# Performance work log

Hardware: AMD Instinct MI355X
Metric: run time of the kernel (lower is better)

## Reference

```python
import jax, jax.numpy as jnp
import numpy as np

BN_EPS = 1e-5
NUM_HEADS = 4
PROJ = 512

def _bn(x, gamma, beta, mean, var):
    # eval-mode BatchNorm1d over last dim
    return (x - mean) * jax.lax.rsqrt(var + BN_EPS) * gamma + beta

def setup_inputs() -> dict:
    key = jax.random.key(0)
    ks = jax.random.split(key, 12)
    B, Tq, Tk, D = 32, 256, 1024, 512
    inp = {
        "s": jax.random.normal(ks[0], (B, Tq, D), jnp.float32),
        "h": jax.random.normal(ks[1], (B, Tk, D), jnp.float32),
        "phi_gamma": jnp.ones((D,), jnp.float32),
        "phi_beta": jnp.zeros((D,), jnp.float32),
        "phi_mean": 0.1 * jax.random.normal(ks[2], (D,), jnp.float32),
        "phi_var": jax.random.uniform(ks[3], (D,), jnp.float32, 0.5, 1.5),
        "W_phi": 0.02 * jax.random.normal(ks[4], (PROJ * NUM_HEADS, D), jnp.float32),
        "psi_gamma": jnp.ones((D,), jnp.float32),
        "psi_beta": jnp.zeros((D,), jnp.float32),
        "psi_mean": 0.1 * jax.random.normal(ks[5], (D,), jnp.float32),
        "psi_var": jax.random.uniform(ks[6], (D,), jnp.float32, 0.5, 1.5),
        "W_psi": 0.02 * jax.random.normal(ks[7], (PROJ, D), jnp.float32),
        "red_gamma": jnp.ones((D * NUM_HEADS,), jnp.float32),
        "red_beta": jnp.zeros((D * NUM_HEADS,), jnp.float32),
        "red_mean": 0.1 * jax.random.normal(ks[8], (D * NUM_HEADS,), jnp.float32),
        "red_var": jax.random.uniform(ks[9], (D * NUM_HEADS,), jnp.float32, 0.5, 1.5),
        "W_red": 0.02 * jax.random.normal(ks[10], (D, D * NUM_HEADS), jnp.float32),
    }
    return inp

def reference(s, h, phi_gamma, phi_beta, phi_mean, phi_var, W_phi,
              psi_gamma, psi_beta, psi_mean, psi_var, W_psi,
              red_gamma, red_beta, red_mean, red_var, W_red):
    B, Tq, _ = s.shape
    # phi: BN + Linear on decoder states -> (B, Tq, H*PROJ)
    ms = _bn(s, phi_gamma, phi_beta, phi_mean, phi_var) @ W_phi.T
    # psi: BN + Linear on encoder states -> (B, Tk, PROJ)
    mh = _bn(h, psi_gamma, psi_beta, psi_mean, psi_var) @ W_psi.T
    # split heads along last dim of ms (matches torch.split order)
    ms4 = ms.reshape(B, Tq, NUM_HEADS, PROJ)
    # unscaled dot-product scores per head: (H, B, Tq, Tk)
    e = jnp.einsum("bqhd,bkd->hbqk", ms4, mh)
    a = jax.nn.softmax(e, axis=-1)
    # context uses the ORIGINAL h (not mh): (B, Tq, H, D) -> concat heads
    ctx = jnp.einsum("hbqk,bkv->bqhv", a, h).reshape(B, Tq, -1)
    # reduce: BN + Linear -> (B, Tq, D)
    c = _bn(ctx, red_gamma, red_beta, red_mean, red_var) @ W_red.T
    return (a, c)
```

## Files before the change

kernel.cpp:

```cpp
#include <hip/hip_runtime.h>

typedef short s8v __attribute__((ext_vector_type(8)));
typedef float f4v __attribute__((ext_vector_type(4)));

static constexpr int Bc = 32, Tq = 256, Tkc = 1024, Dc = 512, Hc = 4;
static constexpr float BN_EPS = 1e-5f;

__device__ inline ushort f2bf(float x) {
    union { float f; unsigned int u; } v; v.f = x;
    unsigned int r = v.u + 0x7fff + ((v.u >> 16) & 1);
    return (ushort)(r >> 16);
}

__global__ __launch_bounds__(256) void fold_bn(
    const float* __restrict__ W, const float* __restrict__ gamma,
    const float* __restrict__ beta, const float* __restrict__ mean,
    const float* __restrict__ var, ushort* __restrict__ Wp,
    float* __restrict__ bias, int K)
{
    int n = blockIdx.x;
    int tid = threadIdx.x;
    float acc = 0.f;
    for (int k = tid; k < K; k += 256) {
        float sc = gamma[k] * rsqrtf(var[k] + BN_EPS);
        float sh = beta[k] - mean[k] * sc;
        float w = W[(long)n * K + k];
        Wp[(long)n * K + k] = f2bf(w * sc);
        acc = fmaf(w, sh, acc);
    }
    __shared__ float red[256];
    red[tid] = acc;
    __syncthreads();
    for (int s = 128; s > 0; s >>= 1) {
        if (tid < s) red[tid] += red[tid + s];
        __syncthreads();
    }
    if (tid == 0) bias[n] = red[0];
}

__global__ __launch_bounds__(256) void f32_to_bf16(
    const float* __restrict__ x, ushort* __restrict__ y)
{
    long i = ((long)blockIdx.x * 256 + threadIdx.x) * 4;
    float4 v = *(const float4*)&x[i];
    ushort4 o = { f2bf(v.x), f2bf(v.y), f2bf(v.z), f2bf(v.w) };
    *(ushort4*)&y[i] = o;
}

__global__ __launch_bounds__(256) void conv_h(
    const float* __restrict__ h, ushort* __restrict__ h_bf,
    ushort* __restrict__ hT)
{
    __shared__ float tl[64][65];
    int b = blockIdx.z, k0 = blockIdx.y * 64, d0 = blockIdx.x * 64;
    int t = threadIdx.x, r = t >> 4, c = (t & 15) * 4;
    const float* hb = h + ((long)b * Tkc + k0) * Dc + d0;
    ushort* sb = h_bf + ((long)b * Tkc + k0) * Dc + d0;
    #pragma unroll
    for (int i = 0; i < 4; i++) {
        int rr = r + i * 16;
        float4 v = *(const float4*)&hb[(long)rr * Dc + c];
        tl[rr][c + 0] = v.x; tl[rr][c + 1] = v.y;
        tl[rr][c + 2] = v.z; tl[rr][c + 3] = v.w;
        ushort4 sv = { f2bf(v.x), f2bf(v.y), f2bf(v.z), f2bf(v.w) };
        *(ushort4*)&sb[(long)rr * Dc + c] = sv;
    }
    __syncthreads();
    ushort* o = hT + ((long)b * Dc + d0) * Tkc + k0;
    #pragma unroll
    for (int i = 0; i < 4; i++) {
        int dr = r + i * 16;
        ushort4 ov = { f2bf(tl[c + 0][dr]), f2bf(tl[c + 1][dr]),
                       f2bf(tl[c + 2][dr]), f2bf(tl[c + 3][dr]) };
        *(ushort4*)&o[(long)dr * Tkc + c] = ov;
    }
}

__global__ __launch_bounds__(256) void init_c(
    float* __restrict__ C, const float* __restrict__ bias)
{
    long i = (long)blockIdx.x * 256 + threadIdx.x;
    int n4 = (int)(i & 127);
    float4 b = ((const float4*)bias)[n4];
    ((float4*)C)[i] = b;
}

typedef __attribute__((address_space(1))) void gvoid;
typedef __attribute__((address_space(3))) void lvoid;

__global__ __launch_bounds__(256, 4) void gemm_mfma(
    const ushort* __restrict__ A, const ushort* __restrict__ B,
    float* __restrict__ Cf, ushort* __restrict__ Cb,
    const float* __restrict__ bias, int atom,
    int K, int lda, int ldb, int ldc,
    long sAh, long sAb, long sBh, long sBb, long sCh, long sCb,
    int nB, int nxs, int zbits)
{
    int bx = blockIdx.x;
    int z = bx & ((1 << zbits) - 1);
    int j2 = bx >> zbits;
    int gx = j2 & ((1 << nxs) - 1);
    int gy = j2 >> nxs;

    int hh = z / nB, bb = z - hh * nB;
    A += hh * sAh + bb * sAb;
    B += hh * sBh + bb * sBb;
    long coff = hh * sCh + bb * sCb;

    __shared__ ushort Als[128 * 64];
    __shared__ ushort Bls[128 * 64];

    int tid = threadIdx.x;
    int l = tid & 63, w = tid >> 6;
    int m0 = gy * 128, n0 = gx * 128;

    const ushort* gA[4]; const ushort* gB[4];
    ushort* lA[4]; ushort* lB[4];
    #pragma unroll
    for (int j = 0; j < 4; j++) {
        int L = (w * 4 + j) * 64 + l;
        int m = L >> 3, c = L & 7;
        int kof = (c ^ ((m >> 1) & 7)) * 8;
        gA[j] = A + (long)(m0 + m) * lda + kof;
        gB[j] = B + (long)(n0 + m) * ldb + kof;
        lA[j] = &Als[(w * 4 + j) * 512];
        lB[j] = &Bls[(w * 4 + j) * 512];
    }

    int wm = (w >> 1) * 64, wn = (w & 1) * 64;
    int fr = l & 15, kc = l >> 4;

    int aidx[2][4], bidx[2][4];
    #pragma unroll
    for (int kk = 0; kk < 2; kk++)
        #pragma unroll
        for (int t = 0; t < 4; t++) {
            int ra = wm + t * 16 + fr;
            aidx[kk][t] = (ra * 8 + ((kk * 4 + kc) ^ ((ra >> 1) & 7))) * 8;
            int rb = wn + t * 16 + fr;
            bidx[kk][t] = (rb * 8 + ((kk * 4 + kc) ^ ((rb >> 1) & 7))) * 8;
        }

    f4v acc[4][4] = {};

    for (int k0 = 0; k0 < K; k0 += 64) {
        #pragma unroll
        for (int j = 0; j < 4; j++) {
            __builtin_amdgcn_global_load_lds((gvoid*)(gA[j] + k0), (lvoid*)lA[j], 16, 0, 0);
            __builtin_amdgcn_global_load_lds((gvoid*)(gB[j] + k0), (lvoid*)lB[j], 16, 0, 0);
        }
        __syncthreads();
        #pragma unroll
        for (int kk = 0; kk < 2; kk++) {
            s8v af[4], bfv[4];
            #pragma unroll
            for (int t = 0; t < 4; t++) af[t]  = *(const s8v*)&Als[aidx[kk][t]];
            #pragma unroll
            for (int t = 0; t < 4; t++) bfv[t] = *(const s8v*)&Bls[bidx[kk][t]];
            #pragma unroll
            for (int i = 0; i < 4; i++)
                #pragma unroll
                for (int jj = 0; jj < 4; jj++)
                    acc[i][jj] = __builtin_amdgcn_mfma_f32_16x16x32_bf16(
                        af[i], bfv[jj], acc[i][jj], 0, 0, 0);
        }
        __syncthreads();
    }

    #pragma unroll
    for (int i = 0; i < 4; i++) {
        #pragma unroll
        for (int jj = 0; jj < 4; jj++) {
            int n = n0 + wn + jj * 16 + fr;
            float bv = bias ? bias[n] : 0.f;
            #pragma unroll
            for (int r = 0; r < 4; r++) {
                int m = m0 + wm + i * 16 + kc * 4 + r;
                float v = acc[i][jj][r] + bv;
                long off = coff + (long)m * ldc + n;
                if (atom)    atomicAdd(&Cf[off], v);
                else if (Cb) Cb[off] = f2bf(v);
                else         Cf[off] = v;
            }
        }
    }
}

__global__ __launch_bounds__(256) void softmax_rows(
    float* __restrict__ E, ushort* __restrict__ Abf)
{
    int wave = threadIdx.x >> 6;
    int lane = threadIdx.x & 63;
    long row = (long)blockIdx.x * 4 + wave;
    float4* rp = (float4*)(E + row * 1024);
    ushort* op = Abf + row * 1024;

    float4 v[4];
    float mx = -3.4e38f;
    #pragma unroll
    for (int i = 0; i < 4; i++) {
        v[i] = rp[lane + (i << 6)];
        mx = fmaxf(mx, fmaxf(fmaxf(v[i].x, v[i].y), fmaxf(v[i].z, v[i].w)));
    }
    #pragma unroll
    for (int o = 32; o > 0; o >>= 1) mx = fmaxf(mx, __shfl_xor(mx, o, 64));

    float sum = 0.f;
    #pragma unroll
    for (int i = 0; i < 4; i++) {
        v[i].x = __expf(v[i].x - mx);
        v[i].y = __expf(v[i].y - mx);
        v[i].z = __expf(v[i].z - mx);
        v[i].w = __expf(v[i].w - mx);
        sum += v[i].x + v[i].y + v[i].z + v[i].w;
    }
    #pragma unroll
    for (int o = 32; o > 0; o >>= 1) sum += __shfl_xor(sum, o, 64);

    float inv = 1.f / sum;
    #pragma unroll
    for (int i = 0; i < 4; i++) {
        v[i].x *= inv; v[i].y *= inv; v[i].z *= inv; v[i].w *= inv;
        rp[lane + (i << 6)] = v[i];
        ushort4 ov = { f2bf(v[i].x), f2bf(v[i].y), f2bf(v[i].z), f2bf(v[i].w) };
        *(ushort4*)&op[(lane + (i << 6)) * 4] = ov;
    }
}

extern "C" void kernel_launch(void* const* d_in, const int* in_sizes, int n_in,
                              void* d_out, int out_size, void* d_ws, size_t ws_size,
                              hipStream_t stream)
{
    const float* s     = (const float*)d_in[0];
    const float* h     = (const float*)d_in[1];
    const float* phi_g = (const float*)d_in[2];
    const float* phi_b = (const float*)d_in[3];
    const float* phi_m = (const float*)d_in[4];
    const float* phi_v = (const float*)d_in[5];
    const float* W_phi = (const float*)d_in[6];
    const float* psi_g = (const float*)d_in[7];
    const float* psi_b = (const float*)d_in[8];
    const float* psi_m = (const float*)d_in[9];
    const float* psi_v = (const float*)d_in[10];
    const float* W_psi = (const float*)d_in[11];
    const float* red_g = (const float*)d_in[12];
    const float* red_b = (const float*)d_in[13];
    const float* red_m = (const float*)d_in[14];
    const float* red_v = (const float*)d_in[15];
    const float* W_red = (const float*)d_in[16];

    float* out_a = (float*)d_out;
    float* out_c = out_a + (long)Hc * Bc * Tq * Tkc;

    char* p = (char*)d_ws;
    ushort* Wphi_b = (ushort*)p;  p += (long)2048 * 512 * 2;
    ushort* Wpsi_b = (ushort*)p;  p += (long)512 * 512 * 2;
    ushort* Wred_b = (ushort*)p;  p += (long)512 * 2048 * 2;
    float* bias_phi = (float*)p;  p += 2048 * 4;
    float* bias_psi = (float*)p;  p += 512 * 4;
    float* bias_red = (float*)p;  p += 512 * 4;
    ushort* s_bf  = (ushort*)p;   p += (long)8192 * 512 * 2;
    ushort* h_bf  = (ushort*)p;   p += (long)32768 * 512 * 2;
    ushort* hT_bf = (ushort*)p;   p += (long)32768 * 512 * 2;
    ushort* ms_bf = (ushort*)p;   p += (long)8192 * 2048 * 2;
    ushort* mh_bf = (ushort*)p;   p += (long)32768 * 512 * 2;
    ushort* a_bf  = ms_bf;
    ushort* ctx_bf = s_bf;

    fold_bn<<<2048, 256, 0, stream>>>(W_phi, phi_g, phi_b, phi_m, phi_v, Wphi_b, bias_phi, 512);
    fold_bn<<<512,  256, 0, stream>>>(W_psi, psi_g, psi_b, psi_m, psi_v, Wpsi_b, bias_psi, 512);
    fold_bn<<<512,  256, 0, stream>>>(W_red, red_g, red_b, red_m, red_v, Wred_b, bias_red, 2048);

    f32_to_bf16<<<4096, 256, 0, stream>>>(s, s_bf);
    conv_h<<<dim3(8, 16, 32), 256, 0, stream>>>(h, h_bf, hT_bf);
    init_c<<<4096, 256, 0, stream>>>(out_c, bias_red);

    gemm_mfma<<<16 * 64, 256, 0, stream>>>(
        s_bf, Wphi_b, nullptr, ms_bf, bias_phi, 0,
        512, 512, 512, 2048, 0, 0, 0, 0, 0, 0, 1, 4, 0);

    gemm_mfma<<<4 * 256, 256, 0, stream>>>(
        h_bf, Wpsi_b, nullptr, mh_bf, bias_psi, 0,
        512, 512, 512, 512, 0, 0, 0, 0, 0, 0, 1, 2, 0);

    gemm_mfma<<<8 * 2 * 128, 256, 0, stream>>>(
        ms_bf, mh_bf, out_a, nullptr, nullptr, 0,
        512, 2048, 512, 1024,
         512,  (long)Tq * 2048,
         0,  (long)Tkc * 512,
         (long)Bc * Tq * Tkc,  (long)Tq * Tkc,
        Bc, 3, 7);

    softmax_rows<<<(Hc * Bc * Tq) / 4, 256, 0, stream>>>(out_a, a_bf);

    gemm_mfma<<<4 * 2 * 128, 256, 0, stream>>>(
        a_bf, hT_bf, nullptr, ctx_bf, nullptr, 0,
        1024, 1024, 1024, 2048,
         (long)Bc * Tq * Tkc,  (long)Tq * Tkc,
         0,  (long)Dc * Tkc,
         512,  (long)Tq * 2048,
        Bc, 2, 7);

    gemm_mfma<<<4 * 64 * 4, 256, 0, stream>>>(
        ctx_bf, Wred_b, out_c, nullptr, nullptr, 1,
        512, 2048, 2048, 512,
         512,  0,
         512,  0,
         0,  0,
        1, 2, 2);
}
```

Before: 524.5 us.

## Replace 128x128 GEMM with 256x256 double-buffered 8-wave MFMA pipeline

Replaces the 128x128-tile, 4-wave GEMM with a 256x256-tile, 8-wave kernel. It double-buffers LDS (128KB), interleaves the global-to-LDS staging of the next K-tile with MFMA quadrants, and uses explicit barriers, vmcnt waits and setprio. All five GEMM launches are re-gridded to match. The larger tiles raise data reuse and hide load latency, but they cut the block count sharply, to 256 blocks for several GEMMs. That risks underfilling the 256 CUs and adds heavy register and LDS pressure.

```diff
diff --git a/kernel.cpp b/kernel.cpp
--- a/kernel.cpp
+++ b/kernel.cpp
@@ -88,7 +88,82 @@
 typedef __attribute__((address_space(1))) void gvoid;
 typedef __attribute__((address_space(3))) void lvoid;
 
-__global__ __launch_bounds__(256, 4) void gemm_mfma(
+#define GLOAD(gp, lp) __builtin_amdgcn_global_load_lds((gvoid*)(gp), (lvoid*)(lp), 16, 0, 0)
+#define BAR() asm volatile("s_barrier" ::: "memory")
+#define WAITV(n) asm volatile("s_waitcnt vmcnt(" #n ")" ::: "memory")
+
+#define STG_A(t, h, bufb) do { \
+    GLOAD(sA + (long)((h) * 128) * lda + (t) * 64, &lds[(bufb) + (h) * 8192 + ldsAc]); \
+    GLOAD(sA + (long)((h) * 128 + 8) * lda + (t) * 64, &lds[(bufb) + (h) * 8192 + ldsAc + 512]); \
+} while (0)
+#define STG_B(t, h, bufb) do { \
+    GLOAD(sB + (long)((h) * 128) * ldb + (t) * 64, &lds[(bufb) + 16384 + (h) * 8192 + ldsBc]); \
+    GLOAD(sB + (long)((h) * 128 + 8) * ldb + (t) * 64, &lds[(bufb) + 16384 + (h) * 8192 + ldsBc + 512]); \
+} while (0)
+
+#define RD_A(mh_, bufb) do { \
+    _Pragma("unroll") \
+    for (int mi = 0; mi < 4; mi++) { \
+        aF[mi][0] = *(const s8v*)&lds[(bufb) + ahalf + ((mh_) * 4 + mi) * 1024 + aoff]; \
+        aF[mi][1] = *(const s8v*)&lds[(bufb) + ahalf + ((mh_) * 4 + mi) * 1024 + (aoff ^ 32)]; \
+    } \
+} while (0)
+#define RD_B(dst, nh_, bufb) do { \
+    _Pragma("unroll") \
+    for (int ni = 0; ni < 2; ni++) { \
+        dst[ni][0] = *(const s8v*)&lds[(bufb) + bhalf + ((nh_) * 2 + ni) * 1024 + aoff]; \
+        dst[ni][1] = *(const s8v*)&lds[(bufb) + bhalf + ((nh_) * 2 + ni) * 1024 + (aoff ^ 32)]; \
+    } \
+} while (0)
+#define MFQ(mh_, nh_, bv) do { \
+    __builtin_amdgcn_s_setprio(1); \
+    _Pragma("unroll") \
+    for (int mi = 0; mi < 4; mi++) \
+        _Pragma("unroll") \
+        for (int ni = 0; ni < 2; ni++) { \
+            acc[(mh_) * 4 + mi][(nh_) * 2 + ni] = __builtin_amdgcn_mfma_f32_16x16x32_bf16( \
+                aF[mi][0], bv[ni][0], acc[(mh_) * 4 + mi][(nh_) * 2 + ni], 0, 0, 0); \
+            acc[(mh_) * 4 + mi][(nh_) * 2 + ni] = __builtin_amdgcn_mfma_f32_16x16x32_bf16( \
+                aF[mi][1], bv[ni][1], acc[(mh_) * 4 + mi][(nh_) * 2 + ni], 0, 0, 0); \
+        } \
+    __builtin_amdgcn_s_setprio(0); \
+} while (0)
+
+#define ITER(T0, PF) do { \
+    const int t0_ = (T0); \
+     \
+    RD_A(0, 0); RD_B(bLo, 0, 0); \
+    STG_B(t0_ + 1, 1, 32768); \
+    BAR(); MFQ(0, 0, bLo); BAR(); \
+     \
+    RD_B(bHi, 1, 0); \
+    STG_A(t0_ + 1, 1, 32768); \
+    BAR(); MFQ(0, 1, bHi); BAR(); \
+     \
+    RD_A(1, 0); \
+    if (PF) STG_B(t0_ + 2, 0, 0); \
+    BAR(); MFQ(1, 0, bLo); BAR(); \
+     \
+    if (PF) { STG_A(t0_ + 2, 0, 0); WAITV(4); } else { WAITV(0); } \
+    BAR(); MFQ(1, 1, bHi); BAR(); \
+     \
+    RD_A(0, 32768); RD_B(bLo, 0, 32768); \
+    if (PF) STG_B(t0_ + 2, 1, 0); \
+    BAR(); MFQ(0, 0, bLo); BAR(); \
+     \
+    RD_B(bHi, 1, 32768); \
+    if (PF) STG_A(t0_ + 2, 1, 0); \
+    BAR(); MFQ(0, 1, bHi); BAR(); \
+     \
+    RD_A(1, 32768); \
+    if (PF) STG_B(t0_ + 3, 0, 32768); \
+    BAR(); MFQ(1, 0, bLo); BAR(); \
+     \
+    if (PF) { STG_A(t0_ + 3, 0, 32768); WAITV(4); } \
+    BAR(); MFQ(1, 1, bHi); BAR(); \
+} while (0)
+
+__global__ __launch_bounds__(512, 2) void gemm256(
     const ushort* __restrict__ A, const ushort* __restrict__ B,
     float* __restrict__ Cf, ushort* __restrict__ Cb,
     const float* __restrict__ bias, int atom,
@@ -96,87 +171,56 @@
     long sAh, long sAb, long sBh, long sBb, long sCh, long sCb,
     int nB, int nxs, int zbits)
 {
+    __shared__ ushort lds[65536];
+
     int bx = blockIdx.x;
     int z = bx & ((1 << zbits) - 1);
     int j2 = bx >> zbits;
     int gx = j2 & ((1 << nxs) - 1);
     int gy = j2 >> nxs;
-
     int hh = z / nB, bb = z - hh * nB;
     A += hh * sAh + bb * sAb;
     B += hh * sBh + bb * sBb;
     long coff = hh * sCh + bb * sCb;
 
-    __shared__ ushort Als[128 * 64];
-    __shared__ ushort Bls[128 * 64];
-
     int tid = threadIdx.x;
-    int l = tid & 63, w = tid >> 6;
-    int m0 = gy * 128, n0 = gx * 128;
-
-    const ushort* gA[4]; const ushort* gB[4];
-    ushort* lA[4]; ushort* lB[4];
-    #pragma unroll
-    for (int j = 0; j < 4; j++) {
-        int L = (w * 4 + j) * 64 + l;
-        int m = L >> 3, c = L & 7;
-        int kof = (c ^ ((m >> 1) & 7)) * 8;
-        gA[j] = A + (long)(m0 + m) * lda + kof;
-        gB[j] = B + (long)(n0 + m) * ldb + kof;
-        lA[j] = &Als[(w * 4 + j) * 512];
-        lB[j] = &Bls[(w * 4 + j) * 512];
-    }
-
-    int wm = (w >> 1) * 64, wn = (w & 1) * 64;
-    int fr = l & 15, kc = l >> 4;
-
-    int aidx[2][4], bidx[2][4];
-    #pragma unroll
-    for (int kk = 0; kk < 2; kk++)
+    int w = tid >> 6, l = tid & 63;
+    int m0 = gy << 8, n0 = gx << 8;
+
+    int skc = ((l & 7) ^ ((l >> 3) & 7)) * 8;
+    const ushort* sA = A + (long)(m0 + w * 16 + (l >> 3)) * lda + skc;
+    const ushort* sB = B + (long)(n0 + w * 16 + (l >> 3)) * ldb + skc;
+    int ldsAc = w * 1024;
+    int ldsBc = w * 1024;
+
+    int fr = l & 15, kc16 = l >> 4;
+    int ahalf = (w >> 2) * 8192;
+    int bhalf = 16384 + ((w & 3) >> 1) * 8192 + (w & 1) * 4096;
+    int aoff = fr * 64 + ((kc16 ^ (fr & 7)) << 3);
+
+    s8v aF[4][2], bLo[2][2], bHi[2][2];
+    f4v acc[8][4] = {};
+
+    STG_A(0, 0, 0); STG_A(0, 1, 0); STG_B(0, 0, 0); STG_B(0, 1, 0);
+    STG_B(1, 0, 32768); STG_A(1, 0, 32768);
+    WAITV(4);
+    BAR();
+
+    int NI = K >> 7;
+    for (int i = 0; i < NI - 1; i++) { ITER(2 * i, 1); }
+    ITER(2 * (NI - 1), 0);
+
+    int wm = (w >> 2) * 128, wn = (w & 3) * 64;
+    #pragma unroll
+    for (int mi = 0; mi < 8; mi++) {
         #pragma unroll
-        for (int t = 0; t < 4; t++) {
-            int ra = wm + t * 16 + fr;
-            aidx[kk][t] = (ra * 8 + ((kk * 4 + kc) ^ ((ra >> 1) & 7))) * 8;
-            int rb = wn + t * 16 + fr;
-            bidx[kk][t] = (rb * 8 + ((kk * 4 + kc) ^ ((rb >> 1) & 7))) * 8;
-        }
-
-    f4v acc[4][4] = {};
-
-    for (int k0 = 0; k0 < K; k0 += 64) {
-        #pragma unroll
-        for (int j = 0; j < 4; j++) {
-            __builtin_amdgcn_global_load_lds((gvoid*)(gA[j] + k0), (lvoid*)lA[j], 16, 0, 0);
-            __builtin_amdgcn_global_load_lds((gvoid*)(gB[j] + k0), (lvoid*)lB[j], 16, 0, 0);
-        }
-        __syncthreads();
-        #pragma unroll
-        for (int kk = 0; kk < 2; kk++) {
-            s8v af[4], bfv[4];
-            #pragma unroll
-            for (int t = 0; t < 4; t++) af[t]  = *(const s8v*)&Als[aidx[kk][t]];
-            #pragma unroll
-            for (int t = 0; t < 4; t++) bfv[t] = *(const s8v*)&Bls[bidx[kk][t]];
-            #pragma unroll
-            for (int i = 0; i < 4; i++)
-                #pragma unroll
-                for (int jj = 0; jj < 4; jj++)
-                    acc[i][jj] = __builtin_amdgcn_mfma_f32_16x16x32_bf16(
-                        af[i], bfv[jj], acc[i][jj], 0, 0, 0);
-        }
-        __syncthreads();
-    }
-
-    #pragma unroll
-    for (int i = 0; i < 4; i++) {
-        #pragma unroll
-        for (int jj = 0; jj < 4; jj++) {
-            int n = n0 + wn + jj * 16 + fr;
+        for (int ni = 0; ni < 4; ni++) {
+            int n = n0 + wn + ni * 16 + fr;
             float bv = bias ? bias[n] : 0.f;
             #pragma unroll
             for (int r = 0; r < 4; r++) {
-                int m = m0 + wm + i * 16 + kc * 4 + r;
-                float v = acc[i][jj][r] + bv;
+                int m = m0 + wm + mi * 16 + kc16 * 4 + r;
+                float v = acc[mi][ni][r] + bv;
                 long off = coff + (long)m * ldc + n;
                 if (atom)    atomicAdd(&Cf[off], v);
                 else if (Cb) Cb[off] = f2bf(v);
@@ -275,37 +319,37 @@
     conv_h<<<dim3(8, 16, 32), 256, 0, stream>>>(h, h_bf, hT_bf);
     init_c<<<4096, 256, 0, stream>>>(out_c, bias_red);
 
-    gemm_mfma<<<16 * 64, 256, 0, stream>>>(
+    gemm256<<<256, 512, 0, stream>>>(
         s_bf, Wphi_b, nullptr, ms_bf, bias_phi, 0,
-        512, 512, 512, 2048, 0, 0, 0, 0, 0, 0, 1, 4, 0);
-
-    gemm_mfma<<<4 * 256, 256, 0, stream>>>(
+        512, 512, 512, 2048, 0, 0, 0, 0, 0, 0, 1, 3, 0);
+
+    gemm256<<<256, 512, 0, stream>>>(
         h_bf, Wpsi_b, nullptr, mh_bf, bias_psi, 0,
-        512, 512, 512, 512, 0, 0, 0, 0, 0, 0, 1, 2, 0);
-
-    gemm_mfma<<<8 * 2 * 128, 256, 0, stream>>>(
+        512, 512, 512, 512, 0, 0, 0, 0, 0, 0, 1, 1, 0);
+
+    gemm256<<<4 * 128, 512, 0, stream>>>(
         ms_bf, mh_bf, out_a, nullptr, nullptr, 0,
         512, 2048, 512, 1024,
          512,  (long)Tq * 2048,
          0,  (long)Tkc * 512,
          (long)Bc * Tq * Tkc,  (long)Tq * Tkc,
-        Bc, 3, 7);
+        Bc, 2, 7);
 
     softmax_rows<<<(Hc * Bc * Tq) / 4, 256, 0, stream>>>(out_a, a_bf);
 
-    gemm_mfma<<<4 * 2 * 128, 256, 0, stream>>>(
+    gemm256<<<2 * 128, 512, 0, stream>>>(
         a_bf, hT_bf, nullptr, ctx_bf, nullptr, 0,
         1024, 1024, 1024, 2048,
          (long)Bc * Tq * Tkc,  (long)Tq * Tkc,
          0,  (long)Dc * Tkc,
          512,  (long)Tq * 2048,
-        Bc, 2, 7);
-
-    gemm_mfma<<<4 * 64 * 4, 256, 0, stream>>>(
+        Bc, 1, 7);
+
+    gemm256<<<32 * 2 * 4, 512, 0, stream>>>(
         ctx_bf, Wred_b, out_c, nullptr, nullptr, 1,
         512, 2048, 2048, 512,
          512,  0,
          512,  0,
          0,  0,
-        1, 2, 2);
-}
+        1, 1, 2);
+}
```

After: 543.5 us. +3.6%, slower.

## Fuse score GEMM with row softmax into one kernel writing fp32 and bf16

Applied to the files above, without the earlier changes.

Replaces the separate score GEMM and softmax pass with a fused kernel. Each 512-thread block computes a 64x1024 score tile across all keys with double-buffered LDS staging, then does the row max/sum reductions in registers and LDS and writes both the fp32 probabilities and the bf16 copy. This avoids writing the fp32 scores and reading them back for softmax. The attention-value and reduction GEMMs are chunked over batch slices sized to the available workspace. In exchange, the large per-block accumulator footprint (4x8 MFMA tiles per wave) and the big LDS allocation limit occupancy, and the epilogue stores are strided and uncoalesced.

```diff
diff --git a/kernel.cpp b/kernel.cpp
--- a/kernel.cpp
+++ b/kernel.cpp
@@ -88,6 +88,10 @@
 typedef __attribute__((address_space(1))) void gvoid;
 typedef __attribute__((address_space(3))) void lvoid;
 
+#define GLOAD(gp, lp) __builtin_amdgcn_global_load_lds((gvoid*)(gp), (lvoid*)(lp), 16, 0, 0)
+#define BAR() asm volatile("s_barrier" ::: "memory")
+#define WAITV0() asm volatile("s_waitcnt vmcnt(0)" ::: "memory")
+
 __global__ __launch_bounds__(256, 4) void gemm_mfma(
     const ushort* __restrict__ A, const ushort* __restrict__ B,
     float* __restrict__ Cf, ushort* __restrict__ Cb,
@@ -146,8 +150,8 @@
     for (int k0 = 0; k0 < K; k0 += 64) {
         #pragma unroll
         for (int j = 0; j < 4; j++) {
-            __builtin_amdgcn_global_load_lds((gvoid*)(gA[j] + k0), (lvoid*)lA[j], 16, 0, 0);
-            __builtin_amdgcn_global_load_lds((gvoid*)(gB[j] + k0), (lvoid*)lB[j], 16, 0, 0);
+            GLOAD(gA[j] + k0, lA[j]);
+            GLOAD(gB[j] + k0, lB[j]);
         }
         __syncthreads();
         #pragma unroll
@@ -186,45 +190,153 @@
     }
 }
 
-__global__ __launch_bounds__(256) void softmax_rows(
-    float* __restrict__ E, ushort* __restrict__ Abf)
-{
-    int wave = threadIdx.x >> 6;
-    int lane = threadIdx.x & 63;
-    long row = (long)blockIdx.x * 4 + wave;
-    float4* rp = (float4*)(E + row * 1024);
-    ushort* op = Abf + row * 1024;
-
-    float4 v[4];
-    float mx = -3.4e38f;
-    #pragma unroll
-    for (int i = 0; i < 4; i++) {
-        v[i] = rp[lane + (i << 6)];
-        mx = fmaxf(mx, fmaxf(fmaxf(v[i].x, v[i].y), fmaxf(v[i].z, v[i].w)));
-    }
-    #pragma unroll
-    for (int o = 32; o > 0; o >>= 1) mx = fmaxf(mx, __shfl_xor(mx, o, 64));
-
-    float sum = 0.f;
-    #pragma unroll
-    for (int i = 0; i < 4; i++) {
-        v[i].x = __expf(v[i].x - mx);
-        v[i].y = __expf(v[i].y - mx);
-        v[i].z = __expf(v[i].z - mx);
-        v[i].w = __expf(v[i].w - mx);
-        sum += v[i].x + v[i].y + v[i].z + v[i].w;
-    }
-    #pragma unroll
-    for (int o = 32; o > 0; o >>= 1) sum += __shfl_xor(sum, o, 64);
-
-    float inv = 1.f / sum;
-    #pragma unroll
-    for (int i = 0; i < 4; i++) {
-        v[i].x *= inv; v[i].y *= inv; v[i].z *= inv; v[i].w *= inv;
-        rp[lane + (i << 6)] = v[i];
-        ushort4 ov = { f2bf(v[i].x), f2bf(v[i].y), f2bf(v[i].z), f2bf(v[i].w) };
-        *(ushort4*)&op[(lane + (i << 6)) * 4] = ov;
-    }
+#define FBUF 34816
+
+#define FSTG(t, bufb) do { \
+    if (w < 4) GLOAD(gAs + (t) * 32, &lds[(bufb) + w * 512]); \
+    _Pragma("unroll") \
+    for (int j = 0; j < 8; j++) \
+        GLOAD(gBs + j * 8192 + (t) * 32, &lds[(bufb) + 2048 + (w * 8 + j) * 512]); \
+} while (0)
+
+#define FCOMP(bufb) do { \
+    s8v aF[4]; \
+    _Pragma("unroll") \
+    for (int mi = 0; mi < 4; mi++) \
+        aF[mi] = *(const s8v*)&lds[(bufb) + mi * 512 + l * 8]; \
+    _Pragma("unroll") \
+    for (int j = 0; j < 8; j++) { \
+        s8v bF = *(const s8v*)&lds[(bufb) + 2048 + (w * 8 + j) * 512 + l * 8]; \
+        _Pragma("unroll") \
+        for (int mi = 0; mi < 4; mi++) \
+            acc[mi][j] = __builtin_amdgcn_mfma_f32_16x16x32_bf16( \
+                aF[mi], bF, acc[mi][j], 0, 0, 0); \
+    } \
+} while (0)
+
+__global__ __launch_bounds__(512, 2) void fused_esm(
+    const ushort* __restrict__ ms, const ushort* __restrict__ mh,
+    float* __restrict__ outA, ushort* __restrict__ aB, int lognb)
+{
+    __shared__ ushort lds[69632];
+
+    int bx = blockIdx.x;
+    int bbl = bx & ((1 << lognb) - 1);
+    int hm = bx >> lognb;
+    int hh = hm >> 2, mt = hm & 3;
+    int nb = 1 << lognb;
+
+    int tid = threadIdx.x;
+    int w = tid >> 6, l = tid & 63;
+
+    const ushort* gAs = ms + ((long)(bbl * 256 + mt * 64 + (w & 3) * 16 + (l & 15))) * 2048
+                           + hh * 512 + ((l >> 4) * 8);
+    const ushort* gBs = mh + ((long)(bbl * 1024 + w * 128 + (l & 15))) * 512
+                           + ((l >> 4) * 8);
+
+    f4v acc[4][8] = {};
+
+    FSTG(0, 0); WAITV0(); BAR();
+    #pragma unroll 1
+    for (int t2 = 0; t2 < 7; ++t2) {
+        FSTG(2 * t2 + 1, FBUF); FCOMP(0);    WAITV0(); BAR();
+        FSTG(2 * t2 + 2, 0);    FCOMP(FBUF); WAITV0(); BAR();
+    }
+    FSTG(15, FBUF); FCOMP(0); WAITV0(); BAR();
+    FCOMP(FBUF);
+
+    __syncthreads();
+    float* red = (float*)lds;
+    int g4 = l >> 4;
+
+    float mxv[4][4];
+    #pragma unroll
+    for (int mi = 0; mi < 4; mi++)
+        #pragma unroll
+        for (int r = 0; r < 4; r++) {
+            float m_ = acc[mi][0][r];
+            #pragma unroll
+            for (int j = 1; j < 8; j++) m_ = fmaxf(m_, acc[mi][j][r]);
+            m_ = fmaxf(m_, __shfl_xor(m_, 1, 64));
+            m_ = fmaxf(m_, __shfl_xor(m_, 2, 64));
+            m_ = fmaxf(m_, __shfl_xor(m_, 4, 64));
+            m_ = fmaxf(m_, __shfl_xor(m_, 8, 64));
+            mxv[mi][r] = m_;
+        }
+    if ((l & 15) == 0) {
+        #pragma unroll
+        for (int mi = 0; mi < 4; mi++)
+            #pragma unroll
+            for (int r = 0; r < 4; r++)
+                red[w * 64 + mi * 16 + g4 * 4 + r] = mxv[mi][r];
+    }
+    __syncthreads();
+    if (tid < 64) {
+        float m_ = red[tid];
+        #pragma unroll
+        for (int ww = 1; ww < 8; ww++) m_ = fmaxf(m_, red[ww * 64 + tid]);
+        red[512 + tid] = m_;
+    }
+    __syncthreads();
+    #pragma unroll
+    for (int mi = 0; mi < 4; mi++) {
+        float4 f = *(const float4*)&red[512 + mi * 16 + g4 * 4];
+        mxv[mi][0] = f.x; mxv[mi][1] = f.y; mxv[mi][2] = f.z; mxv[mi][3] = f.w;
+    }
+
+    float smv[4][4];
+    #pragma unroll
+    for (int mi = 0; mi < 4; mi++)
+        #pragma unroll
+        for (int r = 0; r < 4; r++) {
+            float s_ = 0.f;
+            #pragma unroll
+            for (int j = 0; j < 8; j++) {
+                float e = __expf(acc[mi][j][r] - mxv[mi][r]);
+                acc[mi][j][r] = e;
+                s_ += e;
+            }
+            s_ += __shfl_xor(s_, 1, 64);
+            s_ += __shfl_xor(s_, 2, 64);
+            s_ += __shfl_xor(s_, 4, 64);
+            s_ += __shfl_xor(s_, 8, 64);
+            smv[mi][r] = s_;
+        }
+    if ((l & 15) == 0) {
+        #pragma unroll
+        for (int mi = 0; mi < 4; mi++)
+            #pragma unroll
+            for (int r = 0; r < 4; r++)
+                red[w * 64 + mi * 16 + g4 * 4 + r] = smv[mi][r];
+    }
+    __syncthreads();
+    if (tid < 64) {
+        float s_ = red[tid];
+        #pragma unroll
+        for (int ww = 1; ww < 8; ww++) s_ += red[ww * 64 + tid];
+        red[512 + tid] = 1.f / s_;
+    }
+    __syncthreads();
+    #pragma unroll
+    for (int mi = 0; mi < 4; mi++) {
+        float4 f = *(const float4*)&red[512 + mi * 16 + g4 * 4];
+        smv[mi][0] = f.x; smv[mi][1] = f.y; smv[mi][2] = f.z; smv[mi][3] = f.w;
+    }
+
+    float* oA = outA + ((long)(hh * 32 + bbl) * 256 + mt * 64) * 1024;
+    ushort* oB = aB + ((long)(hh * nb + bbl) * 256 + mt * 64) * 1024;
+    #pragma unroll
+    for (int mi = 0; mi < 4; mi++)
+        #pragma unroll
+        for (int j = 0; j < 8; j++)
+            #pragma unroll
+            for (int r = 0; r < 4; r++) {
+                int rr = mi * 16 + g4 * 4 + r;
+                int cc = w * 128 + j * 16 + (l & 15);
+                float p = acc[mi][j][r] * smv[mi][r];
+                oA[(long)rr * 1024 + cc] = p;
+                oB[(long)rr * 1024 + cc] = f2bf(p);
+            }
 }
 
 extern "C" void kernel_launch(void* const* d_in, const int* in_sizes, int n_in,
@@ -264,8 +376,24 @@
     ushort* hT_bf = (ushort*)p;   p += (long)32768 * 512 * 2;
     ushort* ms_bf = (ushort*)p;   p += (long)8192 * 2048 * 2;
     ushort* mh_bf = (ushort*)p;   p += (long)32768 * 512 * 2;
-    ushort* a_bf  = ms_bf;
-    ushort* ctx_bf = s_bf;
+
+    long avail = (long)ws_size - (p - (char*)d_ws);
+    int S, lognb;
+    ushort *aReg, *ctxReg;
+    if (avail >= (long)64 * 1024 * 1024) {
+        S = 1; lognb = 5;
+        aReg = (ushort*)p;
+        ctxReg = s_bf;
+    } else if (avail >= (long)16 * 1024 * 1024) {
+        S = 2; lognb = 4;
+        aReg = s_bf;
+        ctxReg = (ushort*)p;
+    } else {
+        S = 4; lognb = 3;
+        aReg = s_bf;
+        ctxReg = s_bf + (long)8 * 1024 * 1024;
+    }
+    int nb = 32 / S;
 
     fold_bn<<<2048, 256, 0, stream>>>(W_phi, phi_g, phi_b, phi_m, phi_v, Wphi_b, bias_phi, 512);
     fold_bn<<<512,  256, 0, stream>>>(W_psi, psi_g, psi_b, psi_m, psi_v, Wpsi_b, bias_psi, 512);
@@ -283,29 +411,27 @@
         h_bf, Wpsi_b, nullptr, mh_bf, bias_psi, 0,
         512, 512, 512, 512, 0, 0, 0, 0, 0, 0, 1, 2, 0);
 
-    gemm_mfma<<<8 * 2 * 128, 256, 0, stream>>>(
-        ms_bf, mh_bf, out_a, nullptr, nullptr, 0,
-        512, 2048, 512, 1024,
-         512,  (long)Tq * 2048,
-         0,  (long)Tkc * 512,
-         (long)Bc * Tq * Tkc,  (long)Tq * Tkc,
-        Bc, 3, 7);
-
-    softmax_rows<<<(Hc * Bc * Tq) / 4, 256, 0, stream>>>(out_a, a_bf);
-
-    gemm_mfma<<<4 * 2 * 128, 256, 0, stream>>>(
-        a_bf, hT_bf, nullptr, ctx_bf, nullptr, 0,
-        1024, 1024, 1024, 2048,
-         (long)Bc * Tq * Tkc,  (long)Tq * Tkc,
-         0,  (long)Dc * Tkc,
-         512,  (long)Tq * 2048,
-        Bc, 2, 7);
-
-    gemm_mfma<<<4 * 64 * 4, 256, 0, stream>>>(
-        ctx_bf, Wred_b, out_c, nullptr, nullptr, 1,
-        512, 2048, 2048, 512,
-         512,  0,
-         512,  0,
-         0,  0,
-        1, 2, 2);
-}
+    for (int q = 0; q < S; q++) {
+        fused_esm<<<16 * nb, 512, 0, stream>>>(
+            ms_bf + (long)q * nb * 256 * 2048,
+            mh_bf + (long)q * nb * 1024 * 512,
+            out_a + (long)q * nb * 256 * 1024,
+            aReg, lognb);
+
+        gemm_mfma<<<8 * 4 * nb, 256, 0, stream>>>(
+            aReg, hT_bf + (long)q * nb * 512 * 1024, nullptr, ctxReg, nullptr, 0,
+            1024, 1024, 1024, 2048,
+             (long)nb * 256 * 1024,  (long)256 * 1024,
+             0,  (long)512 * 1024,
+             512,  (long)256 * 2048,
+            nb, 2, lognb + 2);
+
+        gemm_mfma<<<(2 * nb) * 4 * 4, 256, 0, stream>>>(
+            ctxReg, Wred_b, out_c + (long)q * nb * 256 * 512, nullptr, nullptr, 1,
+            512, 2048, 2048, 512,
+             512,  0,
+             512,  0,
+             0,  0,
+            1, 2, 2);
+    }
+}
```

New measurement: 552.4 us. 1.05x slower.
